# Performance work log

Measured on AMD Instinct MI355X. Metric: run time of the kernel, lower is better.

The kernel has to match this reference:

```python
import jax, jax.numpy as jnp
import numpy as np

TOP_K = 8
H, E, I = 2048, 64, 768  # hidden, experts, moe_intermediate


def setup_inputs() -> dict:
    key = jax.random.key(0)
    k1, k2, k3, k4 = jax.random.split(key, 4)
    hidden_states = jax.random.normal(k1, (2, 256, H), dtype=jnp.float32)
    gate_w = jax.random.normal(k2, (E, H), dtype=jnp.float32) * 0.02   # nn.Linear(H, E).weight
    w13 = jax.random.normal(k3, (E, 2 * I, H), dtype=jnp.float32) * 0.02  # [E, 2I, H]
    w2 = jax.random.normal(k4, (E, H, I), dtype=jnp.float32) * 0.02       # [E, H, I]
    return {"hidden_states": hidden_states, "gate_w": gate_w, "w13": w13, "w2": w2}


def reference(hidden_states, gate_w, w13, w2):
    orig_shape = hidden_states.shape
    x = hidden_states.reshape(-1, orig_shape[-1])  # [M, H]
    M = x.shape[0]
    num_experts = gate_w.shape[0]

    # Router: logits -> fp32 softmax -> top-k -> renormalize
    router_logits = x @ gate_w.T  # [M, E]
    routing_weights = jax.nn.softmax(router_logits.astype(jnp.float32), axis=-1)
    topk_w, topk_ids = jax.lax.top_k(routing_weights, TOP_K)  # [M, K]
    topk_w = topk_w / jnp.sum(topk_w, axis=-1, keepdims=True)

    # Scatter top-k weights into a dense [M, E] combine matrix (zeros elsewhere),
    # equivalent to dispatch -> grouped expert FFN -> weighted combine.
    combine = jnp.zeros((M, num_experts), jnp.float32).at[
        jnp.arange(M)[:, None], topk_ids
    ].add(topk_w)

    # Expert FFN: gate/up projection, SiLU-gate, down projection.
    h = jnp.einsum('mh,eih->emi', x, w13)          # [E, M, 2I]
    g, u = jnp.split(h, 2, axis=-1)                # each [E, M, I]
    act = jax.nn.silu(g) * u                       # [E, M, I]
    expert_out = jnp.einsum('emi,ehi->emh', act, w2)  # [E, M, H]

    out = jnp.einsum('emh,me->mh', expert_out, combine)  # weighted combine
    return out.reshape(orig_shape)
```

## Files before the change

### kernel.cpp

```cpp
#include <hip/hip_runtime.h>
#include <hip/hip_bf16.h>

#define H_ 2048
#define E_ 64
#define I_ 768
#define K_ 8
#define GT 5
#define BKF 32

typedef __attribute__((ext_vector_type(8))) __bf16 bf16x8;
typedef __attribute__((ext_vector_type(4))) float f32x4;

__device__ inline unsigned short f2bfbits(float f) {
  unsigned u = __float_as_uint(f);
  u = (u + 0x7fffu + ((u >> 16) & 1u)) >> 16;
  return (unsigned short)u;
}
__device__ inline __bf16 f2bf(float f) {
  union { unsigned short s; __bf16 b; } cv; cv.s = f2bfbits(f); return cv.b;
}
__device__ inline f32x4 mfma16(bf16x8 a, bf16x8 b, f32x4 c) {
  return __builtin_amdgcn_mfma_f32_16x16x32_bf16(a, b, c, 0, 0, 0);
}
__device__ inline bf16x8 pack8(float4 a, float4 b) {
  bf16x8 r;
  r[0] = f2bf(a.x); r[1] = f2bf(a.y); r[2] = f2bf(a.z); r[3] = f2bf(a.w);
  r[4] = f2bf(b.x); r[5] = f2bf(b.y); r[6] = f2bf(b.z); r[7] = f2bf(b.w);
  return r;
}
__device__ inline void dma16(const float* g, float* l) {
  __builtin_amdgcn_global_load_lds(
      (const __attribute__((address_space(1))) float*)g,
      (__attribute__((address_space(3))) float*)l, 16, 0, 0);
}
__device__ inline void fence_sync() {
  asm volatile("" ::: "memory");
  __builtin_amdgcn_s_barrier();
  asm volatile("" ::: "memory");
}

__global__ __launch_bounds__(256) void router_kernel(
    const float* __restrict__ x, const float* __restrict__ gw,
    int* __restrict__ topk_id, float* __restrict__ topk_w,
    __hip_bfloat16* __restrict__ xb) {
  __shared__ float xs[H_];
  __shared__ float probs[E_];
  int m = blockIdx.x;
  const float* xr = x + (size_t)m * H_;
  for (int i = threadIdx.x; i < H_; i += 256) xs[i] = xr[i];
  __syncthreads();
  unsigned short* xbr = reinterpret_cast<unsigned short*>(xb) + (size_t)m * H_;
  for (int i = threadIdx.x; i < H_; i += 256) xbr[i] = f2bfbits(xs[i]);
  int e = threadIdx.x >> 2, part = threadIdx.x & 3;
  const float* gr = gw + (size_t)e * H_ + part * (H_ / 4);
  const float* xx = xs + part * (H_ / 4);
  float s = 0.f;
#pragma unroll 8
  for (int i = 0; i < H_ / 4; ++i) s = fmaf(xx[i], gr[i], s);
  s += __shfl_xor(s, 1);
  s += __shfl_xor(s, 2);
  if (part == 0) probs[e] = s;
  __syncthreads();
  if (threadIdx.x == 0) {
    float mx = -1e30f;
    for (int i = 0; i < E_; ++i) mx = fmaxf(mx, probs[i]);
    float sum = 0.f;
    for (int i = 0; i < E_; ++i) { float p = expf(probs[i] - mx); probs[i] = p; sum += p; }
    float inv = 1.f / sum;
    for (int i = 0; i < E_; ++i) probs[i] *= inv;
    float bw[K_]; int bi[K_]; float wsum = 0.f;
#pragma unroll
    for (int k = 0; k < K_; ++k) {
      float best = -1.f; int b = 0;
      for (int i = 0; i < E_; ++i) if (probs[i] > best) { best = probs[i]; b = i; }
      bw[k] = best; bi[k] = b; wsum += best; probs[b] = -2.f;
    }
    float winv = 1.f / wsum;
#pragma unroll
    for (int k = 0; k < K_; ++k) {
      topk_id[m * K_ + k] = bi[k];
      topk_w[m * K_ + k] = bw[k] * winv;
    }
  }
}

__global__ void zero_cnt_kernel(int* cnt) {
  if (threadIdx.x < E_) cnt[threadIdx.x] = 0;
}

__global__ void scatter_kernel(const int* __restrict__ topk_id, int* cnt,
                               int* perEx, int MK, int M) {
  int idx = blockIdx.x * 256 + threadIdx.x;
  if (idx >= MK) return;
  int e = topk_id[idx];
  int pos = atomicAdd(cnt + e, 1);
  perEx[e * M + pos] = idx;
}

__global__ void scan_kernel(const int* cnt, int* off) {
  if (threadIdx.x == 0) {
    int a = 0;
    for (int e = 0; e < E_; ++e) { off[e] = a; a += cnt[e]; }
    off[E_] = a;
  }
}

__global__ void compact_kernel(const int* __restrict__ cnt, const int* __restrict__ off,
                               const int* __restrict__ perEx,
                               int* __restrict__ entry_mk, int* __restrict__ slot2g, int M) {
  int e = blockIdx.x; int n = cnt[e]; int b = off[e];
  for (int p = threadIdx.x; p < n; p += 256) {
    int mk = perEx[e * M + p];
    entry_mk[b + p] = mk;
    slot2g[mk] = b + p;
  }
}

__global__ __launch_bounds__(256, 2) void gateup_mfma(
    const __hip_bfloat16* __restrict__ xb, const float* __restrict__ w13,
    const int* __restrict__ cnt, const int* __restrict__ off,
    const int* __restrict__ entry_mk, __hip_bfloat16* __restrict__ ACT) {
  __shared__ __align__(16) float lds[2][128 * BKF];
  int e = blockIdx.y;
  int ne = cnt[e];
  if (ne == 0) return;
  int base = off[e];
  int wv = threadIdx.x >> 6, lane = threadIdx.x & 63;
  int i0 = blockIdx.x * 64;
  int col = lane & 15, kq = lane >> 4;
  int myrow = wv * 16 + col;
  int s0 = (2 * kq) ^ (col & 7);
  const float* w13e = w13 + (size_t)e * (2 * I_) * H_;

  const float* dsrc[4];
#pragma unroll
  for (int q = 0; q < 4; ++q) {
    int c = wv * 4 + q;
    int r = 8 * (c & 7) + (lane >> 3);
    int j = (lane & 7) ^ ((lane >> 3) & 7);
    size_t row = (size_t)(i0 + r) + (c >= 8 ? (size_t)I_ : (size_t)0);
    dsrc[q] = w13e + row * H_ + (size_t)j * 4;
  }

  const int NCH = H_ / BKF;
  int ntile = (ne + 15) >> 4;
  for (int tb = 0; tb < ntile; tb += GT) {
    const __hip_bfloat16* arow0[GT];
#pragma unroll
    for (int t = 0; t < GT; ++t) {
      int p = (tb + t) * 16 + col;
      int pc = p < ne ? p : ne - 1;
      int tok = entry_mk[base + pc] >> 3;
      arow0[t] = xb + (size_t)tok * H_ + kq * 8;
    }
    f32x4 accg[GT], accu[GT];
#pragma unroll
    for (int t = 0; t < GT; ++t) {
      accg[t] = (f32x4){0.f, 0.f, 0.f, 0.f};
      accu[t] = (f32x4){0.f, 0.f, 0.f, 0.f};
    }
    bf16x8 aA[GT], aB[GT];
#pragma unroll
    for (int t = 0; t < GT; ++t) aA[t] = *reinterpret_cast<const bf16x8*>(arow0[t]);
#pragma unroll
    for (int q = 0; q < 4; ++q) dma16(dsrc[q], &lds[0][(wv * 4 + q) * 256]);

    auto step = [&](int n, bf16x8 (&ac)[GT], bf16x8 (&an)[GT],
                    const float* ldsC, float* ldsN) {
      if (n + 1 < NCH) {
        size_t ko = (size_t)(n + 1) * BKF;
#pragma unroll
        for (int t = 0; t < GT; ++t)
          an[t] = *reinterpret_cast<const bf16x8*>(arow0[t] + ko);
#pragma unroll
        for (int q = 0; q < 4; ++q)
          dma16(dsrc[q] + ko, ldsN + (wv * 4 + q) * 256);
        asm volatile("s_waitcnt vmcnt(9)" ::: "memory");
      } else {
        asm volatile("s_waitcnt vmcnt(0)" ::: "memory");
      }
      __builtin_amdgcn_sched_barrier(0);
      fence_sync();
      const float4* L = reinterpret_cast<const float4*>(ldsC);
      float4 g0 = L[myrow * 8 + s0];
      float4 g1 = L[myrow * 8 + (s0 ^ 1)];
      float4 u0 = L[(64 + myrow) * 8 + s0];
      float4 u1 = L[(64 + myrow) * 8 + (s0 ^ 1)];
      bf16x8 bg = pack8(g0, g1);
      bf16x8 bu = pack8(u0, u1);
#pragma unroll
      for (int t = 0; t < GT; ++t) {
        accg[t] = mfma16(ac[t], bg, accg[t]);
        accu[t] = mfma16(ac[t], bu, accu[t]);
      }
      asm volatile("s_waitcnt lgkmcnt(0)" ::: "memory");
      __builtin_amdgcn_sched_barrier(0);
      fence_sync();
    };
    for (int n = 0; n < NCH; n += 2) {
      step(n,     aA, aB, lds[0], lds[1]);
      step(n + 1, aB, aA, lds[1], lds[0]);
    }
#pragma unroll
    for (int t = 0; t < GT; ++t) {
#pragma unroll
      for (int r = 0; r < 4; ++r) {
        int m = (tb + t) * 16 + kq * 4 + r;
        if (m < ne) {
          float gv = accg[t][r], uv = accu[t][r];
          float act = gv / (1.f + __expf(-gv)) * uv;
          reinterpret_cast<unsigned short*>(ACT)[(size_t)(base + m) * I_ + i0 + myrow] =
              f2bfbits(act);
        }
      }
    }
  }
}

__global__ __launch_bounds__(256, 2) void down_mfma(
    const __hip_bfloat16* __restrict__ ACT, const float* __restrict__ w2,
    const int* __restrict__ cnt, const int* __restrict__ off,
    float* __restrict__ OUTS) {
  __shared__ __align__(16) float lds[2][64 * BKF];
  int e = blockIdx.y;
  int ne = cnt[e];
  if (ne == 0) return;
  int base = off[e];
  int wv = threadIdx.x >> 6, lane = threadIdx.x & 63;
  int h0 = blockIdx.x * 64;
  int col = lane & 15, kq = lane >> 4;
  int myrow = wv * 16 + col;
  int s0 = (2 * kq) ^ (col & 7);
  const float* w2e = w2 + (size_t)e * H_ * I_;

  const float* dsrc[2];
#pragma unroll
  for (int q = 0; q < 2; ++q) {
    int c = wv * 2 + q;
    int r = 8 * c + (lane >> 3);
    int j = (lane & 7) ^ ((lane >> 3) & 7);
    dsrc[q] = w2e + (size_t)(h0 + r) * I_ + (size_t)j * 4;
  }

  const int NCH = I_ / BKF;
  int ntile = (ne + 15) >> 4;
  for (int tb = 0; tb < ntile; tb += GT) {
    const __hip_bfloat16* arow0[GT];
#pragma unroll
    for (int t = 0; t < GT; ++t) {
      int p = (tb + t) * 16 + col;
      int pc = p < ne ? p : ne - 1;
      arow0[t] = ACT + (size_t)(base + pc) * I_ + kq * 8;
    }
    f32x4 acc[GT];
#pragma unroll
    for (int t = 0; t < GT; ++t) acc[t] = (f32x4){0.f, 0.f, 0.f, 0.f};
    bf16x8 aA[GT], aB[GT];
#pragma unroll
    for (int t = 0; t < GT; ++t) aA[t] = *reinterpret_cast<const bf16x8*>(arow0[t]);
#pragma unroll
    for (int q = 0; q < 2; ++q) dma16(dsrc[q], &lds[0][(wv * 2 + q) * 256]);

    auto step = [&](int n, bf16x8 (&ac)[GT], bf16x8 (&an)[GT],
                    const float* ldsC, float* ldsN) {
      if (n + 1 < NCH) {
        size_t ko = (size_t)(n + 1) * BKF;
#pragma unroll
        for (int t = 0; t < GT; ++t)
          an[t] = *reinterpret_cast<const bf16x8*>(arow0[t] + ko);
#pragma unroll
        for (int q = 0; q < 2; ++q)
          dma16(dsrc[q] + ko, ldsN + (wv * 2 + q) * 256);
        asm volatile("s_waitcnt vmcnt(7)" ::: "memory");
      } else {
        asm volatile("s_waitcnt vmcnt(0)" ::: "memory");
      }
      __builtin_amdgcn_sched_barrier(0);
      fence_sync();
      const float4* L = reinterpret_cast<const float4*>(ldsC);
      float4 w0 = L[myrow * 8 + s0];
      float4 w1 = L[myrow * 8 + (s0 ^ 1)];
      bf16x8 bw = pack8(w0, w1);
#pragma unroll
      for (int t = 0; t < GT; ++t) acc[t] = mfma16(ac[t], bw, acc[t]);
      asm volatile("s_waitcnt lgkmcnt(0)" ::: "memory");
      __builtin_amdgcn_sched_barrier(0);
      fence_sync();
    };
    for (int n = 0; n < NCH; n += 2) {
      step(n,     aA, aB, lds[0], lds[1]);
      step(n + 1, aB, aA, lds[1], lds[0]);
    }
#pragma unroll
    for (int t = 0; t < GT; ++t) {
#pragma unroll
      for (int r = 0; r < 4; ++r) {
        int m = (tb + t) * 16 + kq * 4 + r;
        if (m < ne) {
          OUTS[(size_t)(base + m) * H_ + h0 + myrow] = acc[t][r];
        }
      }
    }
  }
}

__global__ __launch_bounds__(256) void combine_kernel(
    const float* __restrict__ OUTS, const float* __restrict__ topk_w,
    const int* __restrict__ slot2g, float* __restrict__ out) {
  int m = blockIdx.x;
  float w[K_]; int g[K_];
#pragma unroll
  for (int k = 0; k < K_; ++k) { w[k] = topk_w[m * K_ + k]; g[k] = slot2g[m * K_ + k]; }
  for (int h = threadIdx.x; h < H_; h += 256) {
    float s = 0.f;
#pragma unroll
    for (int k = 0; k < K_; ++k) s = fmaf(w[k], OUTS[(size_t)g[k] * H_ + h], s);
    out[(size_t)m * H_ + h] = s;
  }
}

extern "C" void kernel_launch(void* const* d_in, const int* in_sizes, int n_in,
                              void* d_out, int out_size, void* d_ws, size_t ws_size,
                              hipStream_t stream) {
  const float* x   = (const float*)d_in[0];
  const float* gw  = (const float*)d_in[1];
  const float* w13 = (const float*)d_in[2];
  const float* w2  = (const float*)d_in[3];
  float* out = (float*)d_out;

  const int M = in_sizes[0] / H_;
  const int MK = M * K_;

  char* ws = (char*)d_ws;
  size_t o = 0;
  auto alloc = [&](size_t bytes) { size_t r = o; o = (o + bytes + 255) & ~(size_t)255; return r; };
  int*   topk_id  = (int*)(ws + alloc((size_t)MK * 4));
  float* topk_w   = (float*)(ws + alloc((size_t)MK * 4));
  int*   cnt      = (int*)(ws + alloc(E_ * 4));
  int*   off      = (int*)(ws + alloc((E_ + 1) * 4));
  int*   perEx    = (int*)(ws + alloc((size_t)E_ * M * 4));
  int*   entry_mk = (int*)(ws + alloc((size_t)MK * 4));
  int*   slot2g   = (int*)(ws + alloc((size_t)MK * 4));
  __hip_bfloat16* xb  = (__hip_bfloat16*)(ws + alloc((size_t)M * H_ * 2));
  __hip_bfloat16* ACT = (__hip_bfloat16*)(ws + alloc((size_t)MK * I_ * 2));
  float* OUTS     = (float*)(ws + alloc((size_t)MK * H_ * 4));
  (void)ws_size; (void)n_in; (void)out_size;

  router_kernel<<<M, 256, 0, stream>>>(x, gw, topk_id, topk_w, xb);
  zero_cnt_kernel<<<1, 256, 0, stream>>>(cnt);
  scatter_kernel<<<(MK + 255) / 256, 256, 0, stream>>>(topk_id, cnt, perEx, MK, M);
  scan_kernel<<<1, 64, 0, stream>>>(cnt, off);
  compact_kernel<<<E_, 256, 0, stream>>>(cnt, off, perEx, entry_mk, slot2g, M);
  gateup_mfma<<<dim3(I_ / 64, E_), 256, 0, stream>>>(xb, w13, cnt, off, entry_mk, ACT);
  down_mfma<<<dim3(H_ / 64, E_), 256, 0, stream>>>(ACT, w2, cnt, off, OUTS);
  combine_kernel<<<M, 256, 0, stream>>>(OUTS, topk_w, slot2g, out);
}
```

Before: 501.4 us.

## Triple-buffer per-wave LDS weight tiles and drop block barriers in MoE GEMMs

Both expert GEMM kernels now give each wave its own private LDS slice of the weight tile and use a three-stage ring buffer, prefetching two chunks ahead. This removes the two block-wide barriers per K step. LDS reads become inline ds_read_b128 with immediate offsets, and occupancy hints are raised from 2 to 3 blocks per CU. The zero-count kernel is folded into the router kernel to save one launch. The risks are that hand-tuned vmcnt values must exactly match the number of outstanding loads, and that the LDS ring grows.

```diff
diff --git a/kernel.cpp b/kernel.cpp
--- a/kernel.cpp
+++ b/kernel.cpp
@@ -22,10 +22,10 @@
 __device__ inline f32x4 mfma16(bf16x8 a, bf16x8 b, f32x4 c) {
   return __builtin_amdgcn_mfma_f32_16x16x32_bf16(a, b, c, 0, 0, 0);
 }
-__device__ inline bf16x8 pack8(float4 a, float4 b) {
+__device__ inline bf16x8 packv(f32x4 a, f32x4 b) {
   bf16x8 r;
-  r[0] = f2bf(a.x); r[1] = f2bf(a.y); r[2] = f2bf(a.z); r[3] = f2bf(a.w);
-  r[4] = f2bf(b.x); r[5] = f2bf(b.y); r[6] = f2bf(b.z); r[7] = f2bf(b.w);
+  r[0] = f2bf(a[0]); r[1] = f2bf(a[1]); r[2] = f2bf(a[2]); r[3] = f2bf(a[3]);
+  r[4] = f2bf(b[0]); r[5] = f2bf(b[1]); r[6] = f2bf(b[2]); r[7] = f2bf(b[3]);
   return r;
 }
 __device__ inline void dma16(const float* g, float* l) {
@@ -33,19 +33,16 @@
       (const __attribute__((address_space(1))) float*)g,
       (__attribute__((address_space(3))) float*)l, 16, 0, 0);
 }
-__device__ inline void fence_sync() {
-  asm volatile("" ::: "memory");
-  __builtin_amdgcn_s_barrier();
-  asm volatile("" ::: "memory");
-}
+#define SB() __builtin_amdgcn_sched_barrier(0)
 
 __global__ __launch_bounds__(256) void router_kernel(
     const float* __restrict__ x, const float* __restrict__ gw,
     int* __restrict__ topk_id, float* __restrict__ topk_w,
-    __hip_bfloat16* __restrict__ xb) {
+    __hip_bfloat16* __restrict__ xb, int* __restrict__ cnt) {
   __shared__ float xs[H_];
   __shared__ float probs[E_];
   int m = blockIdx.x;
+  if (m == 0 && threadIdx.x < E_) cnt[threadIdx.x] = 0;
   const float* xr = x + (size_t)m * H_;
   for (int i = threadIdx.x; i < H_; i += 256) xs[i] = xr[i];
   __syncthreads();
@@ -84,10 +81,6 @@
   }
 }
 
-__global__ void zero_cnt_kernel(int* cnt) {
-  if (threadIdx.x < E_) cnt[threadIdx.x] = 0;
-}
-
 __global__ void scatter_kernel(const int* __restrict__ topk_id, int* cnt,
                                int* perEx, int MK, int M) {
   int idx = blockIdx.x * 256 + threadIdx.x;
@@ -116,31 +109,29 @@
   }
 }
 
-__global__ __launch_bounds__(256, 2) void gateup_mfma(
+__global__ __launch_bounds__(256, 3) void gateup_mfma(
     const __hip_bfloat16* __restrict__ xb, const float* __restrict__ w13,
     const int* __restrict__ cnt, const int* __restrict__ off,
     const int* __restrict__ entry_mk, __hip_bfloat16* __restrict__ ACT) {
-  __shared__ __align__(16) float lds[2][128 * BKF];
+  __shared__ __align__(16) float lds[3 * 4 * 1024];
   int e = blockIdx.y;
   int ne = cnt[e];
   if (ne == 0) return;
   int base = off[e];
   int wv = threadIdx.x >> 6, lane = threadIdx.x & 63;
-  int i0 = blockIdx.x * 64;
+  int i0 = blockIdx.x * 64 + wv * 16;
   int col = lane & 15, kq = lane >> 4;
-  int myrow = wv * 16 + col;
-  int s0 = (2 * kq) ^ (col & 7);
   const float* w13e = w13 + (size_t)e * (2 * I_) * H_;
 
   const float* dsrc[4];
 #pragma unroll
   for (int q = 0; q < 4; ++q) {
-    int c = wv * 4 + q;
-    int r = 8 * (c & 7) + (lane >> 3);
+    int r = (q & 1) * 8 + (lane >> 3);
     int j = (lane & 7) ^ ((lane >> 3) & 7);
-    size_t row = (size_t)(i0 + r) + (c >= 8 ? (size_t)I_ : (size_t)0);
-    dsrc[q] = w13e + row * H_ + (size_t)j * 4;
-  }
+    size_t row = (size_t)(i0 + r) + ((q >= 2) ? (size_t)I_ : (size_t)0);
+    dsrc[q] = w13e + row * H_ + (size_t)(j * 4);
+  }
+  unsigned laneByte = (unsigned)((col * 8 + ((2 * kq) ^ (col & 7))) * 16);
 
   const int NCH = H_ / BKF;
   int ntile = (ne + 15) >> 4;
@@ -160,47 +151,64 @@
       accu[t] = (f32x4){0.f, 0.f, 0.f, 0.f};
     }
     bf16x8 aA[GT], aB[GT];
+    int bc = 0;
+#pragma unroll
+    for (int q = 0; q < 4; ++q) dma16(dsrc[q], &lds[(0 * 4 + wv) * 1024 + q * 256]);
+    SB();
 #pragma unroll
     for (int t = 0; t < GT; ++t) aA[t] = *reinterpret_cast<const bf16x8*>(arow0[t]);
-#pragma unroll
-    for (int q = 0; q < 4; ++q) dma16(dsrc[q], &lds[0][(wv * 4 + q) * 256]);
-
-    auto step = [&](int n, bf16x8 (&ac)[GT], bf16x8 (&an)[GT],
-                    const float* ldsC, float* ldsN) {
-      if (n + 1 < NCH) {
-        size_t ko = (size_t)(n + 1) * BKF;
+    SB();
+#pragma unroll
+    for (int q = 0; q < 4; ++q) dma16(dsrc[q] + BKF, &lds[(1 * 4 + wv) * 1024 + q * 256]);
+    SB();
+
+    auto stepG = [&](int n, bf16x8 (&ac)[GT], bf16x8 (&an)[GT], int mode) {
+      if (mode == 0) {
+        int bn = (bc == 0) ? 2 : bc - 1;
+        size_t ko = (size_t)(n + 2) * BKF;
+#pragma unroll
+        for (int q = 0; q < 4; ++q)
+          dma16(dsrc[q] + ko, &lds[(bn * 4 + wv) * 1024 + q * 256]);
+        SB();
+      }
+      if (mode <= 1) {
+        size_t ka = (size_t)(n + 1) * BKF;
 #pragma unroll
         for (int t = 0; t < GT; ++t)
-          an[t] = *reinterpret_cast<const bf16x8*>(arow0[t] + ko);
-#pragma unroll
-        for (int q = 0; q < 4; ++q)
-          dma16(dsrc[q] + ko, ldsN + (wv * 4 + q) * 256);
-        asm volatile("s_waitcnt vmcnt(9)" ::: "memory");
-      } else {
-        asm volatile("s_waitcnt vmcnt(0)" ::: "memory");
-      }
-      __builtin_amdgcn_sched_barrier(0);
-      fence_sync();
-      const float4* L = reinterpret_cast<const float4*>(ldsC);
-      float4 g0 = L[myrow * 8 + s0];
-      float4 g1 = L[myrow * 8 + (s0 ^ 1)];
-      float4 u0 = L[(64 + myrow) * 8 + s0];
-      float4 u1 = L[(64 + myrow) * 8 + (s0 ^ 1)];
-      bf16x8 bg = pack8(g0, g1);
-      bf16x8 bu = pack8(u0, u1);
+          an[t] = *reinterpret_cast<const bf16x8*>(arow0[t] + ka);
+        SB();
+      }
+      if (mode == 0)      asm volatile("s_waitcnt vmcnt(13)" ::: "memory");
+      else if (mode == 1) asm volatile("s_waitcnt vmcnt(5)" ::: "memory");
+      else                asm volatile("s_waitcnt vmcnt(0)" ::: "memory");
+      SB();
+      unsigned a0 = (unsigned)(size_t)(&lds[(bc * 4 + wv) * 1024]) + laneByte;
+      unsigned a1 = a0 ^ 16u;
+      f32x4 g0, g1, u0, u1;
+      asm volatile("ds_read_b128 %0, %1" : "=v"(g0) : "v"(a0));
+      asm volatile("ds_read_b128 %0, %1" : "=v"(g1) : "v"(a1));
+      asm volatile("ds_read_b128 %0, %1 offset:2048" : "=v"(u0) : "v"(a0));
+      asm volatile("ds_read_b128 %0, %1 offset:2048" : "=v"(u1) : "v"(a1));
+      asm volatile("s_waitcnt lgkmcnt(0)" ::: "memory");
+      SB();
+      bf16x8 bg = packv(g0, g1);
+      bf16x8 bu = packv(u0, u1);
 #pragma unroll
       for (int t = 0; t < GT; ++t) {
         accg[t] = mfma16(ac[t], bg, accg[t]);
         accu[t] = mfma16(ac[t], bu, accu[t]);
       }
-      asm volatile("s_waitcnt lgkmcnt(0)" ::: "memory");
-      __builtin_amdgcn_sched_barrier(0);
-      fence_sync();
+      bc = (bc == 2) ? 0 : bc + 1;
     };
-    for (int n = 0; n < NCH; n += 2) {
-      step(n,     aA, aB, lds[0], lds[1]);
-      step(n + 1, aB, aA, lds[1], lds[0]);
-    }
+
+#pragma unroll 1
+    for (int n = 0; n + 2 < NCH; n += 2) {
+      stepG(n, aA, aB, 0);
+      stepG(n + 1, aB, aA, 0);
+    }
+    stepG(NCH - 2, aA, aB, 1);
+    stepG(NCH - 1, aB, aA, 2);
+
 #pragma unroll
     for (int t = 0; t < GT; ++t) {
 #pragma unroll
@@ -209,7 +217,7 @@
         if (m < ne) {
           float gv = accg[t][r], uv = accu[t][r];
           float act = gv / (1.f + __expf(-gv)) * uv;
-          reinterpret_cast<unsigned short*>(ACT)[(size_t)(base + m) * I_ + i0 + myrow] =
+          reinterpret_cast<unsigned short*>(ACT)[(size_t)(base + m) * I_ + i0 + col] =
               f2bfbits(act);
         }
       }
@@ -217,30 +225,28 @@
   }
 }
 
-__global__ __launch_bounds__(256, 2) void down_mfma(
+__global__ __launch_bounds__(256, 3) void down_mfma(
     const __hip_bfloat16* __restrict__ ACT, const float* __restrict__ w2,
     const int* __restrict__ cnt, const int* __restrict__ off,
     float* __restrict__ OUTS) {
-  __shared__ __align__(16) float lds[2][64 * BKF];
+  __shared__ __align__(16) float lds[3 * 4 * 512];
   int e = blockIdx.y;
   int ne = cnt[e];
   if (ne == 0) return;
   int base = off[e];
   int wv = threadIdx.x >> 6, lane = threadIdx.x & 63;
-  int h0 = blockIdx.x * 64;
+  int h0 = blockIdx.x * 64 + wv * 16;
   int col = lane & 15, kq = lane >> 4;
-  int myrow = wv * 16 + col;
-  int s0 = (2 * kq) ^ (col & 7);
   const float* w2e = w2 + (size_t)e * H_ * I_;
 
   const float* dsrc[2];
 #pragma unroll
   for (int q = 0; q < 2; ++q) {
-    int c = wv * 2 + q;
-    int r = 8 * c + (lane >> 3);
+    int r = q * 8 + (lane >> 3);
     int j = (lane & 7) ^ ((lane >> 3) & 7);
-    dsrc[q] = w2e + (size_t)(h0 + r) * I_ + (size_t)j * 4;
-  }
+    dsrc[q] = w2e + (size_t)(h0 + r) * I_ + (size_t)(j * 4);
+  }
+  unsigned laneByte = (unsigned)((col * 8 + ((2 * kq) ^ (col & 7))) * 16);
 
   const int NCH = I_ / BKF;
   int ntile = (ne + 15) >> 4;
@@ -256,48 +262,65 @@
 #pragma unroll
     for (int t = 0; t < GT; ++t) acc[t] = (f32x4){0.f, 0.f, 0.f, 0.f};
     bf16x8 aA[GT], aB[GT];
+    int bc = 0;
+#pragma unroll
+    for (int q = 0; q < 2; ++q) dma16(dsrc[q], &lds[(0 * 4 + wv) * 512 + q * 256]);
+    SB();
 #pragma unroll
     for (int t = 0; t < GT; ++t) aA[t] = *reinterpret_cast<const bf16x8*>(arow0[t]);
-#pragma unroll
-    for (int q = 0; q < 2; ++q) dma16(dsrc[q], &lds[0][(wv * 2 + q) * 256]);
-
-    auto step = [&](int n, bf16x8 (&ac)[GT], bf16x8 (&an)[GT],
-                    const float* ldsC, float* ldsN) {
-      if (n + 1 < NCH) {
-        size_t ko = (size_t)(n + 1) * BKF;
+    SB();
+#pragma unroll
+    for (int q = 0; q < 2; ++q) dma16(dsrc[q] + BKF, &lds[(1 * 4 + wv) * 512 + q * 256]);
+    SB();
+
+    auto stepD = [&](int n, bf16x8 (&ac)[GT], bf16x8 (&an)[GT], int mode) {
+      if (mode == 0) {
+        int bn = (bc == 0) ? 2 : bc - 1;
+        size_t ko = (size_t)(n + 2) * BKF;
+#pragma unroll
+        for (int q = 0; q < 2; ++q)
+          dma16(dsrc[q] + ko, &lds[(bn * 4 + wv) * 512 + q * 256]);
+        SB();
+      }
+      if (mode <= 1) {
+        size_t ka = (size_t)(n + 1) * BKF;
 #pragma unroll
         for (int t = 0; t < GT; ++t)
-          an[t] = *reinterpret_cast<const bf16x8*>(arow0[t] + ko);
-#pragma unroll
-        for (int q = 0; q < 2; ++q)
-          dma16(dsrc[q] + ko, ldsN + (wv * 2 + q) * 256);
-        asm volatile("s_waitcnt vmcnt(7)" ::: "memory");
-      } else {
-        asm volatile("s_waitcnt vmcnt(0)" ::: "memory");
-      }
-      __builtin_amdgcn_sched_barrier(0);
-      fence_sync();
-      const float4* L = reinterpret_cast<const float4*>(ldsC);
-      float4 w0 = L[myrow * 8 + s0];
-      float4 w1 = L[myrow * 8 + (s0 ^ 1)];
-      bf16x8 bw = pack8(w0, w1);
+          an[t] = *reinterpret_cast<const bf16x8*>(arow0[t] + ka);
+        SB();
+      }
+      if (mode == 0)      asm volatile("s_waitcnt vmcnt(9)" ::: "memory");
+      else if (mode == 1) asm volatile("s_waitcnt vmcnt(5)" ::: "memory");
+      else                asm volatile("s_waitcnt vmcnt(0)" ::: "memory");
+      SB();
+      unsigned a0 = (unsigned)(size_t)(&lds[(bc * 4 + wv) * 512]) + laneByte;
+      unsigned a1 = a0 ^ 16u;
+      f32x4 w0, w1;
+      asm volatile("ds_read_b128 %0, %1" : "=v"(w0) : "v"(a0));
+      asm volatile("ds_read_b128 %0, %1" : "=v"(w1) : "v"(a1));
+      asm volatile("s_waitcnt lgkmcnt(0)" ::: "memory");
+      SB();
+      bf16x8 bw = packv(w0, w1);
 #pragma unroll
       for (int t = 0; t < GT; ++t) acc[t] = mfma16(ac[t], bw, acc[t]);
-      asm volatile("s_waitcnt lgkmcnt(0)" ::: "memory");
-      __builtin_amdgcn_sched_barrier(0);
-      fence_sync();
+      bc = (bc == 2) ? 0 : bc + 1;
     };
-    for (int n = 0; n < NCH; n += 2) {
-      step(n,     aA, aB, lds[0], lds[1]);
-      step(n + 1, aB, aA, lds[1], lds[0]);
-    }
+
+#pragma unroll 1
+    for (int n = 0; n + 2 < NCH; n += 2) {
+      stepD(n, aA, aB, 0);
+      stepD(n + 1, aB, aA, 0);
+    }
+    stepD(NCH - 2, aA, aB, 1);
+    stepD(NCH - 1, aB, aA, 2);
+
 #pragma unroll
     for (int t = 0; t < GT; ++t) {
 #pragma unroll
       for (int r = 0; r < 4; ++r) {
         int m = (tb + t) * 16 + kq * 4 + r;
         if (m < ne) {
-          OUTS[(size_t)(base + m) * H_ + h0 + myrow] = acc[t][r];
+          OUTS[(size_t)(base + m) * H_ + h0 + col] = acc[t][r];
         }
       }
     }
@@ -346,8 +369,7 @@
   float* OUTS     = (float*)(ws + alloc((size_t)MK * H_ * 4));
   (void)ws_size; (void)n_in; (void)out_size;
 
-  router_kernel<<<M, 256, 0, stream>>>(x, gw, topk_id, topk_w, xb);
-  zero_cnt_kernel<<<1, 256, 0, stream>>>(cnt);
+  router_kernel<<<M, 256, 0, stream>>>(x, gw, topk_id, topk_w, xb, cnt);
   scatter_kernel<<<(MK + 255) / 256, 256, 0, stream>>>(topk_id, cnt, perEx, MK, M);
   scan_kernel<<<1, 64, 0, stream>>>(cnt, off);
   compact_kernel<<<E_, 256, 0, stream>>>(cnt, off, perEx, entry_mk, slot2g, M);
```

Result: faster. 469.0 us (-6.5%).
